# Performance work log

Hardware: AMD Instinct MI355X
Metric: run time of the kernel (lower is better)

Reference implementation:

```python
import jax, jax.numpy as jnp
import numpy as np

N, B, C, H = 2048, 2, 1024, 16
HD = C // H


def setup_inputs() -> dict:
    key = jax.random.key(0)
    ks = jax.random.split(key, 11)
    s = 0.02
    return {
        "query": jax.random.normal(ks[0], (N, B, C), jnp.float32),
        "key": jax.random.normal(ks[1], (N, B, C), jnp.float32),
        "value": jax.random.normal(ks[2], (B, N, C), jnp.float32),
        "num_heads": H,
        "Wq": jax.random.normal(ks[3], (C, C), jnp.float32) * s,
        "bq": jnp.zeros((C,), jnp.float32),
        "Wk": jax.random.normal(ks[4], (C, HD), jnp.float32) * s,
        "bk": jnp.zeros((HD,), jnp.float32),
        "Wv": jax.random.normal(ks[5], (C, HD), jnp.float32) * s,
        "bv": jnp.zeros((HD,), jnp.float32),
        "Wp": jax.random.normal(ks[6], (C, C), jnp.float32) * s,
        "bp": jnp.zeros((C,), jnp.float32),
    }


def reference(query, key, value, num_heads, Wq, bq, Wk, bk, Wv, bv, Wp, bp):
    # query/key arrive seq-first (N,B,C); permute to batch-first as in torch code
    k_in = jnp.transpose(key, (1, 0, 2))    # (B, Nk, C)
    q_in = jnp.transpose(query, (1, 0, 2))  # (B, Nq, C)
    Bsz, Nq, Cd = q_in.shape
    hd = Cd // num_heads
    scale = hd ** -0.5

    # shared single K/V head (MQA)
    k = k_in @ Wk + bk                      # (B, Nk, hd)
    v = value @ Wv + bv                     # (B, Nk, hd)
    q = (q_in @ Wq + bq).reshape(Bsz, Nq, num_heads, hd)
    q = jnp.transpose(q, (0, 2, 1, 3)) * scale  # (B, H, Nq, hd)

    attn = jnp.einsum('bhqd,bkd->bhqk', q, k)   # (B, H, Nq, Nk)
    attn = jax.nn.softmax(attn, axis=-1)
    x = jnp.einsum('bhqk,bkd->bhqd', attn, v)   # (B, H, Nq, hd)
    x = jnp.transpose(x, (0, 2, 1, 3)).reshape(Bsz, Nq, Cd)
    x = x @ Wp + bp
    return jnp.transpose(x, (1, 0, 2))          # (Nq, B, C)
```

## Files before the change

### kernel.cpp

```cpp
#include <hip/hip_runtime.h>
#include <hip/hip_bf16.h>

#define DI __device__ __forceinline__

typedef float f32x4 __attribute__((ext_vector_type(4)));
typedef float f32x16 __attribute__((ext_vector_type(16)));
typedef short s16x8 __attribute__((ext_vector_type(8)));
typedef unsigned short u16x4 __attribute__((ext_vector_type(4)));
typedef unsigned long long u64;


DI unsigned short f2bf(float x) {
  union { float f; unsigned u; } v; v.f = x;
  unsigned r = 0x7fffu + ((v.u >> 16) & 1u);
  return (unsigned short)((v.u + r) >> 16);
}

DI unsigned cvtpk(float lo, float hi) {
  unsigned u;
  asm("v_cvt_pk_bf16_f32 %0, %1, %2" : "=v"(u) : "v"(lo), "v"(hi));
  return u;
}

DI f32x16 zero16() {
  f32x16 z;
#pragma unroll
  for (int i = 0; i < 16; ++i) z[i] = 0.f;
  return z;
}

DI float max16(const f32x16& a) {
  float m0 = fmaxf(a[0], a[1]),  m1 = fmaxf(a[2], a[3]);
  float m2 = fmaxf(a[4], a[5]),  m3 = fmaxf(a[6], a[7]);
  float m4 = fmaxf(a[8], a[9]),  m5 = fmaxf(a[10], a[11]);
  float m6 = fmaxf(a[12], a[13]), m7 = fmaxf(a[14], a[15]);
  m0 = fmaxf(m0, m1); m2 = fmaxf(m2, m3); m4 = fmaxf(m4, m5); m6 = fmaxf(m6, m7);
  return fmaxf(fmaxf(m0, m2), fmaxf(m4, m6));
}

DI float sum16(const f32x16& a) {
  float s0 = a[0] + a[1],  s1 = a[2] + a[3];
  float s2 = a[4] + a[5],  s3 = a[6] + a[7];
  float s4 = a[8] + a[9],  s5 = a[10] + a[11];
  float s6 = a[12] + a[13], s7 = a[14] + a[15];
  s0 += s1; s2 += s3; s4 += s5; s6 += s7;
  return (s0 + s2) + (s4 + s6);
}

DI void gll16(const void* g, void* l) {
  __builtin_amdgcn_global_load_lds(
      (const __attribute__((address_space(1))) void*)g,
      (__attribute__((address_space(3))) void*)l, 16, 0, 0);
}

DI f32x16 mfma32(s16x8 a, s16x8 b, f32x16 c) {
  return __builtin_amdgcn_mfma_f32_32x32x16_bf16(a, b, c, 0, 0, 0);
}

DI f32x4 mfma16(s16x8 a, s16x8 b, f32x4 c) {
  return __builtin_amdgcn_mfma_f32_16x16x32_bf16(a, b, c, 0, 0, 0);
}

__global__ __launch_bounds__(256) void wconv_kernel(
    const float* __restrict__ Wq, const float* __restrict__ Wk,
    const float* __restrict__ Wv, const float* __restrict__ Wp,
    unsigned short* __restrict__ WqT, unsigned short* __restrict__ WkT,
    unsigned short* __restrict__ WvT, unsigned short* __restrict__ WpT)
{
  int bid = blockIdx.x;
  const float* W; unsigned short* WT; int Ncols; int base;
  if (bid < 512)       { W = Wq; WT = WqT; Ncols = 1024; base = bid; }
  else if (bid < 1024) { W = Wp; WT = WpT; Ncols = 1024; base = bid - 512; }
  else if (bid < 1056) { W = Wk; WT = WkT; Ncols = 64;   base = bid - 1024; }
  else                 { W = Wv; WT = WvT; Ncols = 64;   base = bid - 1056; }
  int nb = base >> 5, kb = base & 31;
  int n = nb * 64 + (threadIdx.x & 63);
  int k = kb * 32 + (threadIdx.x >> 6) * 8;
  float f[8];
#pragma unroll
  for (int i = 0; i < 8; ++i) f[i] = W[(size_t)(k + i) * Ncols + n];
  union { unsigned u[4]; s16x8 v; } x;
#pragma unroll
  for (int i = 0; i < 4; ++i) x.u[i] = cvtpk(f[2 * i], f[2 * i + 1]);
  *(s16x8*)(WT + (size_t)n * 1024 + k) = x.v;
}

__global__ __launch_bounds__(256) void cvt3_kernel(
    const float* __restrict__ q, const float* __restrict__ k,
    const float* __restrict__ v, unsigned short* __restrict__ qbf,
    unsigned short* __restrict__ kbf, unsigned short* __restrict__ vbf)
{
  int gid = blockIdx.x * 256 + threadIdx.x;
  int which = gid >> 19;
  int idx = gid & 524287;
  int row = idx >> 7;
  int c8 = (idx & 127) << 3;
  const float* src; unsigned short* dst; size_t soff;
  if (which == 0)      { src = q; dst = qbf; }
  else if (which == 1) { src = k; dst = kbf; }
  else                 { src = v; dst = vbf; }
  if (which < 2) {
    int b = row >> 11, n = row & 2047;
    soff = ((size_t)n * 2 + b) * 1024 + c8;
  } else {
    soff = (size_t)row * 1024 + c8;
  }
  f32x4 v0 = *(const f32x4*)(src + soff);
  f32x4 v1 = *(const f32x4*)(src + soff + 4);
  union { unsigned u[4]; s16x8 v; } x;
  x.u[0] = cvtpk(v0.x, v0.y); x.u[1] = cvtpk(v0.z, v0.w);
  x.u[2] = cvtpk(v1.x, v1.y); x.u[3] = cvtpk(v1.z, v1.w);
  *(s16x8*)(dst + (size_t)row * 1024 + c8) = x.v;
}

template<int BM, int BN, int MODE, int KSPLIT>
__global__ __launch_bounds__(256) void gemm16_kernel(
    const unsigned short* __restrict__ A1, const unsigned short* __restrict__ A2,
    const unsigned short* __restrict__ B1, const unsigned short* __restrict__ B2,
    const float* __restrict__ bias, void* __restrict__ Cpv, float scale)
{
  __shared__ unsigned short Asub[BM * 64];
  __shared__ unsigned short Bsub[BN * 64];

  const int tid = threadIdx.x;
  const int lane = tid & 63, wave = tid >> 6;
  const int l16 = lane & 15, kq = lane >> 4;
  const int wr = wave >> 1, wc = wave & 1;
  constexpr int WROWS = BM / 2, WCOLS = BN / 2;
  constexpr int MI = WROWS / 16, NJ = WCOLS / 16;

  const unsigned short* A = A1; const unsigned short* Bt = B1;
  int sel = 0;
  if constexpr (MODE == 1) {
    sel = blockIdx.y;
    if (sel) { A = A2; Bt = B2; }
  }
  const int row0 = blockIdx.x * BM;
  const int col0 = (MODE == 1) ? 0 : blockIdx.y * BN;
  const int kt0 = (KSPLIT > 1) ? blockIdx.z * (16 / KSPLIT) : 0;
  const int kt1 = kt0 + 16 / KSPLIT;

  f32x4 acc[MI][NJ];
#pragma unroll
  for (int mi = 0; mi < MI; ++mi)
#pragma unroll
    for (int nj = 0; nj < NJ; ++nj) acc[mi][nj] = f32x4{0.f, 0.f, 0.f, 0.f};

  for (int kt = kt0; kt < kt1; ++kt) {
    const int k0 = kt * 64;
    __syncthreads();
#pragma unroll
    for (int i = 0; i < BM / 32; ++i) {
      int o = i * 4096 + tid * 16;
      int r = o >> 7, c = (o & 127) >> 1;
      gll16(A + (size_t)(row0 + r) * 1024 + k0 + c,
            (char*)Asub + i * 4096 + wave * 1024);
    }
#pragma unroll
    for (int i = 0; i < BN / 32; ++i) {
      int o = i * 4096 + tid * 16;
      int r = o >> 7, c = (o & 127) >> 1;
      gll16(Bt + (size_t)(col0 + r) * 1024 + k0 + c,
            (char*)Bsub + i * 4096 + wave * 1024);
    }
    __syncthreads();
#pragma unroll
    for (int ks = 0; ks < 2; ++ks) {
      s16x8 af[MI]; s16x8 bfr[NJ];
#pragma unroll
      for (int mi = 0; mi < MI; ++mi)
        af[mi] = *(const s16x8*)(Asub + (wr * WROWS + mi * 16 + l16) * 64 + ks * 32 + kq * 8);
#pragma unroll
      for (int nj = 0; nj < NJ; ++nj)
        bfr[nj] = *(const s16x8*)(Bsub + (wc * WCOLS + nj * 16 + l16) * 64 + ks * 32 + kq * 8);
#pragma unroll
      for (int mi = 0; mi < MI; ++mi)
#pragma unroll
        for (int nj = 0; nj < NJ; ++nj)
          acc[mi][nj] = mfma16(af[mi], bfr[nj], acc[mi][nj]);
    }
  }

#pragma unroll
  for (int mi = 0; mi < MI; ++mi)
#pragma unroll
  for (int nj = 0; nj < NJ; ++nj) {
    int col = col0 + wc * WCOLS + nj * 16 + l16;
    int rowb = row0 + wr * WROWS + mi * 16 + kq * 4;
    float bv = (MODE == 1) ? 0.f : bias[col];
#pragma unroll
    for (int r = 0; r < 4; ++r) {
      int row = rowb + r;
      float val = acc[mi][nj][r] + bv;
      if constexpr (MODE == 0) {
        ((unsigned short*)Cpv)[(size_t)row * 1024 + col] = f2bf(val * scale);
      } else if constexpr (MODE == 1) {
        ((float*)Cpv)[(((size_t)blockIdx.z * 2 + sel) * 4096 + row) * 64 + col] = val;
      } else {
        ((float*)Cpv)[(size_t)(row & 2047) * 2048 + (size_t)(row >> 11) * 1024 + col] = val;
      }
    }
  }
}

__global__ __launch_bounds__(256) void kvreduce_kernel(
    const float* __restrict__ part, const float* __restrict__ bk,
    const float* __restrict__ bv, unsigned short* __restrict__ kproj,
    unsigned short* __restrict__ vprojT)
{
  int gid = blockIdx.x * 256 + threadIdx.x;
  int kv = gid >> 18;
  int rem = gid & 262143;
  int row = rem >> 6, col = rem & 63;
  float s = 0.f;
#pragma unroll
  for (int z = 0; z < 4; ++z)
    s += part[(((size_t)z * 2 + kv) * 4096 + row) * 64 + col];
  s += (kv ? bv : bk)[col];
  if (kv == 0)
    kproj[(size_t)row * 64 + col] = f2bf(s);
  else
    vprojT[(size_t)(row >> 11) * 131072 + (size_t)col * 2048 + (row & 2047)] = f2bf(s);
}

__global__ __launch_bounds__(512, 4) void attn_kernel(
    const unsigned short* __restrict__ qp, const unsigned short* __restrict__ kp,
    const unsigned short* __restrict__ vpt, unsigned short* __restrict__ xout)
{
  constexpr int KSTR = 72;
  __shared__ unsigned short SM[36864];
#define KBUF(c, hh) (SM + ((c) * 2 + (hh)) * (64 * KSTR))
#define VBUF(c, hh) (SM + 18432 + ((c) * 2 + (hh)) * (64 * KSTR))

  const int tid = threadIdx.x;
  const int lane = tid & 63, wave = tid >> 6;
  const int lq = lane & 31, hi = lane >> 5;
  const int qsub = wave & 3, half = wave >> 2;
  const int b = blockIdx.y >> 4, h = blockIdx.y & 15;
  const int q0 = blockIdx.x * 128 + qsub * 32;
  const size_t qrow = (size_t)(b * 2048 + q0 + lq);

  s16x8 qf[4];
#pragma unroll
  for (int s = 0; s < 4; ++s)
    qf[s] = *(const s16x8*)(qp + qrow * 1024 + h * 64 + s * 16 + hi * 8);

  f32x16 xacc0 = zero16(), xacc1 = zero16();
  float mrun = -1e30f, ssum = 0.f;

  const unsigned short* kb = kp + (size_t)b * (2048 * 64);
  const unsigned short* vb = vpt + (size_t)b * (64 * 2048);

  const int srow = tid >> 3;
  const int scol = (tid & 7) * 8;

  s16x8 kA, kB, vA, vB;
  {
    kA = *(const s16x8*)(kb + (size_t)srow * 64 + scol);
    kB = *(const s16x8*)(kb + (size_t)(16 * 64 + srow) * 64 + scol);
    vA = *(const s16x8*)(vb + (size_t)srow * 2048 + scol);
    vB = *(const s16x8*)(vb + (size_t)srow * 2048 + 16 * 64 + scol);
    *(s16x8*)(KBUF(0, 0) + srow * KSTR + scol) = kA;
    *(s16x8*)(KBUF(0, 1) + srow * KSTR + scol) = kB;
    *(s16x8*)(VBUF(0, 0) + srow * KSTR + scol) = vA;
    *(s16x8*)(VBUF(0, 1) + srow * KSTR + scol) = vB;
  }
  int cur = 0;

  for (int it = 0; it < 16; ++it) {
    __syncthreads();
    if (it + 1 < 16) {
      kA = *(const s16x8*)(kb + (size_t)((it + 1) * 64 + srow) * 64 + scol);
      kB = *(const s16x8*)(kb + (size_t)((it + 17) * 64 + srow) * 64 + scol);
      vA = *(const s16x8*)(vb + (size_t)srow * 2048 + (it + 1) * 64 + scol);
      vB = *(const s16x8*)(vb + (size_t)srow * 2048 + (it + 17) * 64 + scol);
    }
    const unsigned short* Kc = KBUF(cur, half);
    const unsigned short* Vc = VBUF(cur, half);

    f32x16 sacc0 = zero16(), sacc1 = zero16();
    __builtin_amdgcn_s_setprio(1);
#pragma unroll
    for (int s = 0; s < 4; ++s) {
      int c = s * 16 + hi * 8;
      s16x8 kf0 = *(const s16x8*)(Kc + lq * KSTR + c);
      s16x8 kf1 = *(const s16x8*)(Kc + (32 + lq) * KSTR + c);
      sacc0 = mfma32(kf0, qf[s], sacc0);
      sacc1 = mfma32(kf1, qf[s], sacc1);
    }
    __builtin_amdgcn_s_setprio(0);

    float tm = fmaxf(max16(sacc0), max16(sacc1));
    tm = fmaxf(tm, __shfl_xor(tm, 32));
    if (!__all(tm <= mrun + 8.f)) {
      float mnew = fmaxf(mrun, tm);
      float alpha = __builtin_amdgcn_exp2f(mrun - mnew);
      ssum *= alpha;
#pragma unroll
      for (int e = 0; e < 16; ++e) { xacc0[e] *= alpha; xacc1[e] *= alpha; }
      mrun = mnew;
    }
    f32x16 p0, p1;
#pragma unroll
    for (int e = 0; e < 16; ++e) p0[e] = __builtin_amdgcn_exp2f(sacc0[e] - mrun);
#pragma unroll
    for (int e = 0; e < 16; ++e) p1[e] = __builtin_amdgcn_exp2f(sacc1[e] - mrun);
    float tsum = sum16(p0) + sum16(p1);
    tsum += __shfl_xor(tsum, 32);
    ssum += tsum;

    s16x8 pb[4];
#pragma unroll
    for (int grp = 0; grp < 4; ++grp) {
      const f32x16& pp = (grp < 2) ? p0 : p1;
      const int eb = (grp & 1) * 8;
      unsigned A  = cvtpk(pp[eb + 0], pp[eb + 1]);
      unsigned Bw = cvtpk(pp[eb + 2], pp[eb + 3]);
      unsigned Cw = cvtpk(pp[eb + 4], pp[eb + 5]);
      unsigned Dw = cvtpk(pp[eb + 6], pp[eb + 7]);
      unsigned rA = (unsigned)__shfl_xor((int)(hi ? A : Cw), 32);
      unsigned rB = (unsigned)__shfl_xor((int)(hi ? Bw : Dw), 32);
      union { unsigned u[4]; s16x8 v; } pk_;
      pk_.u[0] = hi ? rA : A;
      pk_.u[1] = hi ? rB : Bw;
      pk_.u[2] = hi ? Cw : rA;
      pk_.u[3] = hi ? Dw : rB;
      pb[grp] = pk_.v;
    }

    __builtin_amdgcn_s_setprio(1);
#pragma unroll
    for (int kvs = 0; kvs < 4; ++kvs) {
      int c = kvs * 16 + hi * 8;
      s16x8 vf0 = *(const s16x8*)(Vc + lq * KSTR + c);
      s16x8 vf1 = *(const s16x8*)(Vc + (32 + lq) * KSTR + c);
      xacc0 = mfma32(vf0, pb[kvs], xacc0);
      xacc1 = mfma32(vf1, pb[kvs], xacc1);
    }
    __builtin_amdgcn_s_setprio(0);

    if (it + 1 < 16) {
      *(s16x8*)(KBUF(cur ^ 1, 0) + srow * KSTR + scol) = kA;
      *(s16x8*)(KBUF(cur ^ 1, 1) + srow * KSTR + scol) = kB;
      *(s16x8*)(VBUF(cur ^ 1, 0) + srow * KSTR + scol) = vA;
      *(s16x8*)(VBUF(cur ^ 1, 1) + srow * KSTR + scol) = vB;
      cur ^= 1;
    }
  }

  __syncthreads();
  float* msc = (float*)SM;
  const int mi_ = (qsub * 64 + lane) * 37;
  if (half == 1) {
#pragma unroll
    for (int e = 0; e < 16; ++e) { msc[mi_ + e] = xacc0[e]; msc[mi_ + 16 + e] = xacc1[e]; }
    msc[mi_ + 32] = mrun;
    msc[mi_ + 33] = ssum;
  }
  __syncthreads();
  if (half == 0) {
    float pm = msc[mi_ + 32], ps = msc[mi_ + 33];
    float mf = fmaxf(mrun, pm);
    float aa = __builtin_amdgcn_exp2f(mrun - mf);
    float bb = __builtin_amdgcn_exp2f(pm - mf);
    float inv = 1.0f / (ssum * aa + ps * bb);
#pragma unroll
    for (int dj = 0; dj < 2; ++dj) {
      const f32x16 xa = dj ? xacc1 : xacc0;
#pragma unroll
      for (int g = 0; g < 4; ++g) {
        u16x4 o4;
#pragma unroll
        for (int r = 0; r < 4; ++r) {
          int e = g * 4 + r;
          float merged = xa[e] * aa + msc[mi_ + dj * 16 + e] * bb;
          o4[r] = f2bf(merged * inv);
        }
        int d0 = dj * 32 + 8 * g + 4 * hi;
        *(u16x4*)(xout + qrow * 1024 + h * 64 + d0) = o4;
      }
    }
  }
#undef KBUF
#undef VBUF
}

extern "C" void kernel_launch(void* const* d_in, const int* in_sizes, int n_in,
                              void* d_out, int out_size, void* d_ws, size_t ws_size,
                              hipStream_t stream)
{
  const float* query = (const float*)d_in[0];
  const float* key   = (const float*)d_in[1];
  const float* value = (const float*)d_in[2];
  const float* Wq = (const float*)d_in[4];
  const float* bq = (const float*)d_in[5];
  const float* Wk = (const float*)d_in[6];
  const float* bk = (const float*)d_in[7];
  const float* Wv = (const float*)d_in[8];
  const float* bv = (const float*)d_in[9];
  const float* Wp = (const float*)d_in[10];
  const float* bp = (const float*)d_in[11];

  char* ws = (char*)d_ws;
  unsigned short* WqT    = (unsigned short*)(ws);
  unsigned short* WpT    = (unsigned short*)(ws + (2u << 20));
  unsigned short* WkT    = (unsigned short*)(ws + (4u << 20));
  unsigned short* WvT    = (unsigned short*)(ws + (4u << 20) + (128u << 10));
  unsigned short* kproj  = (unsigned short*)(ws + (5u << 20));
  unsigned short* vprojT = (unsigned short*)(ws + (5u << 20) + (512u << 10));
  unsigned short* qproj  = (unsigned short*)(ws + (6u << 20));
  unsigned short* xbuf   = (unsigned short*)(ws + (15u << 20));
  float*          part   = (float*)xbuf;
  unsigned short* vbf    = (unsigned short*)(ws + (24u << 20));
  unsigned short* qbf    = (unsigned short*)d_out;
  unsigned short* kbf    = (unsigned short*)d_out + 4194304;

  wconv_kernel<<<dim3(1088), 256, 0, stream>>>(Wq, Wk, Wv, Wp, WqT, WkT, WvT, WpT);
  cvt3_kernel<<<dim3(6144), 256, 0, stream>>>(query, key, value, qbf, kbf, vbf);

  const float qscale = 0.18033688011112042f;
  gemm16_kernel<64, 64, 0, 1><<<dim3(64, 16), 256, 0, stream>>>(
      qbf, qbf, WqT, WqT, bq, qproj, qscale);
  gemm16_kernel<64, 64, 1, 4><<<dim3(64, 2, 4), 256, 0, stream>>>(
      kbf, vbf, WkT, WvT, nullptr, part, 1.0f);
  kvreduce_kernel<<<dim3(2048), 256, 0, stream>>>(part, bk, bv, kproj, vprojT);
  attn_kernel<<<dim3(16, 32), 512, 0, stream>>>(qproj, kproj, vprojT, xbuf);
  gemm16_kernel<64, 64, 2, 1><<<dim3(64, 16), 256, 0, stream>>>(
      xbuf, xbuf, WpT, WpT, bp, d_out, 1.0f);
}
```

Measured before the change: 122.2 us.

## Fuse K/V bf16 conversion into KV GEMM, double-buffer GEMMs, retile attention

The separate fp32-to-bf16 conversion of key and value is removed. A new gemmkv_kernel loads fp32 activations, converts them in registers and writes them to LDS, with a register-prefetched double buffer. The Q and output projection GEMMs now use 128x64 tiles with double-buffered global_load_lds staging. The attention kernel processes 32 keys per iteration with a smaller LDS footprint so the occupancy hint can rise from 4 to 6 blocks. It also interleaves exp/pack with the PV MFMAs, uses v_max3 for the row max, and starts the running max at 0 instead of -1e30. That last change relies on the lazy-rescale threshold and adds some numeric risk if scores fall far below zero.

```diff
diff --git a/kernel.cpp b/kernel.cpp
--- a/kernel.cpp
+++ b/kernel.cpp
@@ -22,6 +22,12 @@
   return u;
 }
 
+DI float max3f(float a, float b, float c) {
+  float d;
+  asm("v_max3_f32 %0, %1, %2, %3" : "=v"(d) : "v"(a), "v"(b), "v"(c));
+  return d;
+}
+
 DI f32x16 zero16() {
   f32x16 z;
 #pragma unroll
@@ -29,22 +35,15 @@
   return z;
 }
 
-DI float max16(const f32x16& a) {
-  float m0 = fmaxf(a[0], a[1]),  m1 = fmaxf(a[2], a[3]);
-  float m2 = fmaxf(a[4], a[5]),  m3 = fmaxf(a[6], a[7]);
-  float m4 = fmaxf(a[8], a[9]),  m5 = fmaxf(a[10], a[11]);
-  float m6 = fmaxf(a[12], a[13]), m7 = fmaxf(a[14], a[15]);
-  m0 = fmaxf(m0, m1); m2 = fmaxf(m2, m3); m4 = fmaxf(m4, m5); m6 = fmaxf(m6, m7);
-  return fmaxf(fmaxf(m0, m2), fmaxf(m4, m6));
-}
-
-DI float sum16(const f32x16& a) {
-  float s0 = a[0] + a[1],  s1 = a[2] + a[3];
-  float s2 = a[4] + a[5],  s3 = a[6] + a[7];
-  float s4 = a[8] + a[9],  s5 = a[10] + a[11];
-  float s6 = a[12] + a[13], s7 = a[14] + a[15];
-  s0 += s1; s2 += s3; s4 += s5; s6 += s7;
-  return (s0 + s2) + (s4 + s6);
+DI float max16_3(const f32x16& a) {
+  float m0 = max3f(a[0], a[1], a[2]);
+  float m1 = max3f(a[3], a[4], a[5]);
+  float m2 = max3f(a[6], a[7], a[8]);
+  float m3 = max3f(a[9], a[10], a[11]);
+  float m4 = max3f(a[12], a[13], a[14]);
+  float n0 = max3f(m0, m1, m2);
+  float n1 = max3f(m3, m4, a[15]);
+  return fmaxf(n0, n1);
 }
 
 DI void gll16(const void* g, void* l) {
@@ -85,121 +84,196 @@
   *(s16x8*)(WT + (size_t)n * 1024 + k) = x.v;
 }
 
-__global__ __launch_bounds__(256) void cvt3_kernel(
-    const float* __restrict__ q, const float* __restrict__ k,
-    const float* __restrict__ v, unsigned short* __restrict__ qbf,
-    unsigned short* __restrict__ kbf, unsigned short* __restrict__ vbf)
+__global__ __launch_bounds__(256) void cvt1_kernel(
+    const float* __restrict__ q, unsigned short* __restrict__ qbf)
 {
   int gid = blockIdx.x * 256 + threadIdx.x;
-  int which = gid >> 19;
-  int idx = gid & 524287;
-  int row = idx >> 7;
-  int c8 = (idx & 127) << 3;
-  const float* src; unsigned short* dst; size_t soff;
-  if (which == 0)      { src = q; dst = qbf; }
-  else if (which == 1) { src = k; dst = kbf; }
-  else                 { src = v; dst = vbf; }
-  if (which < 2) {
-    int b = row >> 11, n = row & 2047;
-    soff = ((size_t)n * 2 + b) * 1024 + c8;
-  } else {
-    soff = (size_t)row * 1024 + c8;
-  }
-  f32x4 v0 = *(const f32x4*)(src + soff);
-  f32x4 v1 = *(const f32x4*)(src + soff + 4);
+  int row = gid >> 7;
+  int c8 = (gid & 127) << 3;
+  int b = row >> 11, n = row & 2047;
+  size_t soff = ((size_t)n * 2 + b) * 1024 + c8;
+  f32x4 v0 = *(const f32x4*)(q + soff);
+  f32x4 v1 = *(const f32x4*)(q + soff + 4);
   union { unsigned u[4]; s16x8 v; } x;
   x.u[0] = cvtpk(v0.x, v0.y); x.u[1] = cvtpk(v0.z, v0.w);
   x.u[2] = cvtpk(v1.x, v1.y); x.u[3] = cvtpk(v1.z, v1.w);
-  *(s16x8*)(dst + (size_t)row * 1024 + c8) = x.v;
-}
-
-template<int BM, int BN, int MODE, int KSPLIT>
+  *(s16x8*)(qbf + (size_t)row * 1024 + c8) = x.v;
+}
+
+template<int MODE>
 __global__ __launch_bounds__(256) void gemm16_kernel(
-    const unsigned short* __restrict__ A1, const unsigned short* __restrict__ A2,
-    const unsigned short* __restrict__ B1, const unsigned short* __restrict__ B2,
+    const unsigned short* __restrict__ A, const unsigned short* __restrict__ Bt,
     const float* __restrict__ bias, void* __restrict__ Cpv, float scale)
 {
-  __shared__ unsigned short Asub[BM * 64];
-  __shared__ unsigned short Bsub[BN * 64];
+  __shared__ __align__(16) unsigned short Asub[2][128 * 64];
+  __shared__ __align__(16) unsigned short Bsub[2][64 * 64];
 
   const int tid = threadIdx.x;
   const int lane = tid & 63, wave = tid >> 6;
   const int l16 = lane & 15, kq = lane >> 4;
   const int wr = wave >> 1, wc = wave & 1;
-  constexpr int WROWS = BM / 2, WCOLS = BN / 2;
-  constexpr int MI = WROWS / 16, NJ = WCOLS / 16;
-
-  const unsigned short* A = A1; const unsigned short* Bt = B1;
-  int sel = 0;
-  if constexpr (MODE == 1) {
-    sel = blockIdx.y;
-    if (sel) { A = A2; Bt = B2; }
-  }
-  const int row0 = blockIdx.x * BM;
-  const int col0 = (MODE == 1) ? 0 : blockIdx.y * BN;
-  const int kt0 = (KSPLIT > 1) ? blockIdx.z * (16 / KSPLIT) : 0;
-  const int kt1 = kt0 + 16 / KSPLIT;
-
-  f32x4 acc[MI][NJ];
-#pragma unroll
-  for (int mi = 0; mi < MI; ++mi)
-#pragma unroll
-    for (int nj = 0; nj < NJ; ++nj) acc[mi][nj] = f32x4{0.f, 0.f, 0.f, 0.f};
-
-  for (int kt = kt0; kt < kt1; ++kt) {
+  const int row0 = blockIdx.x * 128;
+  const int col0 = blockIdx.y * 64;
+
+  f32x4 acc[4][2];
+#pragma unroll
+  for (int mi = 0; mi < 4; ++mi)
+#pragma unroll
+    for (int nj = 0; nj < 2; ++nj) acc[mi][nj] = f32x4{0.f, 0.f, 0.f, 0.f};
+
+  auto STAGE = [&](int bf, int kt) {
     const int k0 = kt * 64;
-    __syncthreads();
-#pragma unroll
-    for (int i = 0; i < BM / 32; ++i) {
+#pragma unroll
+    for (int i = 0; i < 4; ++i) {
       int o = i * 4096 + tid * 16;
       int r = o >> 7, c = (o & 127) >> 1;
       gll16(A + (size_t)(row0 + r) * 1024 + k0 + c,
-            (char*)Asub + i * 4096 + wave * 1024);
-    }
-#pragma unroll
-    for (int i = 0; i < BN / 32; ++i) {
+            (char*)Asub[bf] + i * 4096 + wave * 1024);
+    }
+#pragma unroll
+    for (int i = 0; i < 2; ++i) {
       int o = i * 4096 + tid * 16;
       int r = o >> 7, c = (o & 127) >> 1;
       gll16(Bt + (size_t)(col0 + r) * 1024 + k0 + c,
-            (char*)Bsub + i * 4096 + wave * 1024);
+            (char*)Bsub[bf] + i * 4096 + wave * 1024);
+    }
+  };
+
+  STAGE(0, 0);
+  __syncthreads();
+  int cur = 0;
+  for (int kt = 0; kt < 16; ++kt) {
+    if (kt + 1 < 16) STAGE(cur ^ 1, kt + 1);
+#pragma unroll
+    for (int ks = 0; ks < 2; ++ks) {
+      s16x8 af[4]; s16x8 bf2[2];
+#pragma unroll
+      for (int mi = 0; mi < 4; ++mi)
+        af[mi] = *(const s16x8*)(Asub[cur] + (wr * 64 + mi * 16 + l16) * 64 + ks * 32 + kq * 8);
+#pragma unroll
+      for (int nj = 0; nj < 2; ++nj)
+        bf2[nj] = *(const s16x8*)(Bsub[cur] + (wc * 32 + nj * 16 + l16) * 64 + ks * 32 + kq * 8);
+#pragma unroll
+      for (int mi = 0; mi < 4; ++mi)
+#pragma unroll
+        for (int nj = 0; nj < 2; ++nj)
+          acc[mi][nj] = mfma16(af[mi], bf2[nj], acc[mi][nj]);
     }
     __syncthreads();
-#pragma unroll
-    for (int ks = 0; ks < 2; ++ks) {
-      s16x8 af[MI]; s16x8 bfr[NJ];
-#pragma unroll
-      for (int mi = 0; mi < MI; ++mi)
-        af[mi] = *(const s16x8*)(Asub + (wr * WROWS + mi * 16 + l16) * 64 + ks * 32 + kq * 8);
-#pragma unroll
-      for (int nj = 0; nj < NJ; ++nj)
-        bfr[nj] = *(const s16x8*)(Bsub + (wc * WCOLS + nj * 16 + l16) * 64 + ks * 32 + kq * 8);
-#pragma unroll
-      for (int mi = 0; mi < MI; ++mi)
-#pragma unroll
-        for (int nj = 0; nj < NJ; ++nj)
-          acc[mi][nj] = mfma16(af[mi], bfr[nj], acc[mi][nj]);
-    }
-  }
-
-#pragma unroll
-  for (int mi = 0; mi < MI; ++mi)
-#pragma unroll
-  for (int nj = 0; nj < NJ; ++nj) {
-    int col = col0 + wc * WCOLS + nj * 16 + l16;
-    int rowb = row0 + wr * WROWS + mi * 16 + kq * 4;
-    float bv = (MODE == 1) ? 0.f : bias[col];
+    cur ^= 1;
+  }
+
+#pragma unroll
+  for (int mi = 0; mi < 4; ++mi)
+#pragma unroll
+  for (int nj = 0; nj < 2; ++nj) {
+    int col = col0 + wc * 32 + nj * 16 + l16;
+    int rowb = row0 + wr * 64 + mi * 16 + kq * 4;
+    float bv = bias[col];
 #pragma unroll
     for (int r = 0; r < 4; ++r) {
       int row = rowb + r;
       float val = acc[mi][nj][r] + bv;
       if constexpr (MODE == 0) {
         ((unsigned short*)Cpv)[(size_t)row * 1024 + col] = f2bf(val * scale);
-      } else if constexpr (MODE == 1) {
-        ((float*)Cpv)[(((size_t)blockIdx.z * 2 + sel) * 4096 + row) * 64 + col] = val;
       } else {
         ((float*)Cpv)[(size_t)(row & 2047) * 2048 + (size_t)(row >> 11) * 1024 + col] = val;
       }
     }
+  }
+}
+
+__global__ __launch_bounds__(256) void gemmkv_kernel(
+    const float* __restrict__ Akey, const float* __restrict__ Aval,
+    const unsigned short* __restrict__ Wk, const unsigned short* __restrict__ Wv,
+    float* __restrict__ part)
+{
+  __shared__ __align__(16) unsigned short Asub[2][64 * 64];
+  __shared__ __align__(16) unsigned short Bsub[2][64 * 64];
+
+  const int tid = threadIdx.x;
+  const int lane = tid & 63, wave = tid >> 6;
+  const int l16 = lane & 15, kq = lane >> 4;
+  const int wr = wave >> 1, wc = wave & 1;
+  const int sel = blockIdx.y;
+  const float* Af = sel ? Aval : Akey;
+  const unsigned short* Bt = sel ? Wv : Wk;
+  const int row0 = blockIdx.x * 64;
+  const int kt0 = blockIdx.z * 4, kt1 = kt0 + 4;
+
+  const int ar = tid >> 2, ac = (tid & 3) * 16;
+  const int gm = row0 + ar;
+  const size_t grow = sel ? (size_t)gm * 1024
+                          : (size_t)((gm & 2047) * 2 + (gm >> 11)) * 1024;
+
+  auto LOADA = [&](int kt, f32x4* a4) {
+#pragma unroll
+    for (int i = 0; i < 4; ++i)
+      a4[i] = *(const f32x4*)(Af + grow + kt * 64 + ac + i * 4);
+  };
+  auto WRITEA = [&](int bf, const f32x4* a4) {
+    union { unsigned u[8]; s16x8 v[2]; } x;
+#pragma unroll
+    for (int i = 0; i < 4; ++i) {
+      x.u[2 * i]     = cvtpk(a4[i].x, a4[i].y);
+      x.u[2 * i + 1] = cvtpk(a4[i].z, a4[i].w);
+    }
+    *(s16x8*)(Asub[bf] + ar * 64 + ac)     = x.v[0];
+    *(s16x8*)(Asub[bf] + ar * 64 + ac + 8) = x.v[1];
+  };
+  auto STAGEB = [&](int bf, int kt) {
+#pragma unroll
+    for (int i = 0; i < 2; ++i) {
+      int o = i * 4096 + tid * 16;
+      int r = o >> 7, c = (o & 127) >> 1;
+      gll16(Bt + (size_t)r * 1024 + kt * 64 + c,
+            (char*)Bsub[bf] + i * 4096 + wave * 1024);
+    }
+  };
+
+  f32x4 acc[2][2];
+#pragma unroll
+  for (int mi = 0; mi < 2; ++mi)
+#pragma unroll
+    for (int nj = 0; nj < 2; ++nj) acc[mi][nj] = f32x4{0.f, 0.f, 0.f, 0.f};
+
+  f32x4 a4[4];
+  LOADA(kt0, a4);
+  STAGEB(0, kt0);
+  WRITEA(0, a4);
+  __syncthreads();
+  int cur = 0;
+  for (int kt = kt0; kt < kt1; ++kt) {
+    if (kt + 1 < kt1) { LOADA(kt + 1, a4); STAGEB(cur ^ 1, kt + 1); }
+#pragma unroll
+    for (int ks = 0; ks < 2; ++ks) {
+      s16x8 af[2]; s16x8 bf2[2];
+#pragma unroll
+      for (int mi = 0; mi < 2; ++mi)
+        af[mi] = *(const s16x8*)(Asub[cur] + (wr * 32 + mi * 16 + l16) * 64 + ks * 32 + kq * 8);
+#pragma unroll
+      for (int nj = 0; nj < 2; ++nj)
+        bf2[nj] = *(const s16x8*)(Bsub[cur] + (wc * 32 + nj * 16 + l16) * 64 + ks * 32 + kq * 8);
+#pragma unroll
+      for (int mi = 0; mi < 2; ++mi)
+#pragma unroll
+        for (int nj = 0; nj < 2; ++nj)
+          acc[mi][nj] = mfma16(af[mi], bf2[nj], acc[mi][nj]);
+    }
+    if (kt + 1 < kt1) WRITEA(cur ^ 1, a4);
+    __syncthreads();
+    cur ^= 1;
+  }
+
+#pragma unroll
+  for (int mi = 0; mi < 2; ++mi)
+#pragma unroll
+  for (int nj = 0; nj < 2; ++nj) {
+    int col = wc * 32 + nj * 16 + l16;
+    int rowb = row0 + wr * 32 + mi * 16 + kq * 4;
+#pragma unroll
+    for (int r = 0; r < 4; ++r)
+      part[(((size_t)blockIdx.z * 2 + sel) * 4096 + rowb + r) * 64 + col] = acc[mi][nj][r];
   }
 }
 
@@ -223,14 +297,13 @@
     vprojT[(size_t)(row >> 11) * 131072 + (size_t)col * 2048 + (row & 2047)] = f2bf(s);
 }
 
-__global__ __launch_bounds__(512, 4) void attn_kernel(
+__global__ __launch_bounds__(512, 6) void attn_kernel(
     const unsigned short* __restrict__ qp, const unsigned short* __restrict__ kp,
     const unsigned short* __restrict__ vpt, unsigned short* __restrict__ xout)
 {
-  constexpr int KSTR = 72;
-  __shared__ unsigned short SM[36864];
-#define KBUF(c, hh) (SM + ((c) * 2 + (hh)) * (64 * KSTR))
-#define VBUF(c, hh) (SM + 18432 + ((c) * 2 + (hh)) * (64 * KSTR))
+  __shared__ __align__(16) unsigned short SM[19456];
+#define KOFF(c, hh) (SM + (c) * 9728 + (hh) * 2304)
+#define VOFF(c, hh) (SM + (c) * 9728 + 4608 + (hh) * 2560)
 
   const int tid = threadIdx.x;
   const int lane = tid & 63, wave = tid >> 6;
@@ -246,51 +319,42 @@
     qf[s] = *(const s16x8*)(qp + qrow * 1024 + h * 64 + s * 16 + hi * 8);
 
   f32x16 xacc0 = zero16(), xacc1 = zero16();
-  float mrun = -1e30f, ssum = 0.f;
-
-  const unsigned short* kb = kp + (size_t)b * (2048 * 64);
-  const unsigned short* vb = vpt + (size_t)b * (64 * 2048);
-
-  const int srow = tid >> 3;
-  const int scol = (tid & 7) * 8;
-
-  s16x8 kA, kB, vA, vB;
-  {
-    kA = *(const s16x8*)(kb + (size_t)srow * 64 + scol);
-    kB = *(const s16x8*)(kb + (size_t)(16 * 64 + srow) * 64 + scol);
-    vA = *(const s16x8*)(vb + (size_t)srow * 2048 + scol);
-    vB = *(const s16x8*)(vb + (size_t)srow * 2048 + 16 * 64 + scol);
-    *(s16x8*)(KBUF(0, 0) + srow * KSTR + scol) = kA;
-    *(s16x8*)(KBUF(0, 1) + srow * KSTR + scol) = kB;
-    *(s16x8*)(VBUF(0, 0) + srow * KSTR + scol) = vA;
-    *(s16x8*)(VBUF(0, 1) + srow * KSTR + scol) = vB;
-  }
+  float mrun = 0.f, ssum = 0.f;
+
+  const int sh = tid >> 8;
+  const int kidx = tid & 255;
+  const int krow = kidx >> 3, kcol = (kidx & 7) * 8;
+  const int vrow = kidx >> 2, vcol = (kidx & 3) * 8;
+  const unsigned short* kg = kp + (size_t)b * (2048 * 64) + (size_t)(sh * 1024 + krow) * 64 + kcol;
+  const unsigned short* vg = vpt + (size_t)b * (64 * 2048) + (size_t)vrow * 2048 + sh * 1024 + vcol;
+  unsigned short* kd0 = KOFF(0, sh) + krow * 72 + kcol;
+  unsigned short* vd0 = VOFF(0, sh) + vrow * 40 + vcol;
+
+  s16x8 kr = *(const s16x8*)kg;
+  s16x8 vr = *(const s16x8*)vg;
+  *(s16x8*)kd0 = kr;
+  *(s16x8*)vd0 = vr;
   int cur = 0;
 
-  for (int it = 0; it < 16; ++it) {
+  for (int it = 0; it < 32; ++it) {
     __syncthreads();
-    if (it + 1 < 16) {
-      kA = *(const s16x8*)(kb + (size_t)((it + 1) * 64 + srow) * 64 + scol);
-      kB = *(const s16x8*)(kb + (size_t)((it + 17) * 64 + srow) * 64 + scol);
-      vA = *(const s16x8*)(vb + (size_t)srow * 2048 + (it + 1) * 64 + scol);
-      vB = *(const s16x8*)(vb + (size_t)srow * 2048 + (it + 17) * 64 + scol);
-    }
-    const unsigned short* Kc = KBUF(cur, half);
-    const unsigned short* Vc = VBUF(cur, half);
-
-    f32x16 sacc0 = zero16(), sacc1 = zero16();
+    if (it + 1 < 32) {
+      kr = *(const s16x8*)(kg + (size_t)(it + 1) * 2048);
+      vr = *(const s16x8*)(vg + (it + 1) * 32);
+    }
+    const unsigned short* Kc = KOFF(cur, half);
+    const unsigned short* Vc = VOFF(cur, half);
+
+    f32x16 sacc = zero16();
     __builtin_amdgcn_s_setprio(1);
 #pragma unroll
     for (int s = 0; s < 4; ++s) {
-      int c = s * 16 + hi * 8;
-      s16x8 kf0 = *(const s16x8*)(Kc + lq * KSTR + c);
-      s16x8 kf1 = *(const s16x8*)(Kc + (32 + lq) * KSTR + c);
-      sacc0 = mfma32(kf0, qf[s], sacc0);
-      sacc1 = mfma32(kf1, qf[s], sacc1);
+      s16x8 kf = *(const s16x8*)(Kc + lq * 72 + s * 16 + hi * 8);
+      sacc = mfma32(kf, qf[s], sacc);
     }
     __builtin_amdgcn_s_setprio(0);
 
-    float tm = fmaxf(max16(sacc0), max16(sacc1));
+    float tm = max16_3(sacc);
     tm = fmaxf(tm, __shfl_xor(tm, 32));
     if (!__all(tm <= mrun + 8.f)) {
       float mnew = fmaxf(mrun, tm);
@@ -300,24 +364,24 @@
       for (int e = 0; e < 16; ++e) { xacc0[e] *= alpha; xacc1[e] *= alpha; }
       mrun = mnew;
     }
-    f32x16 p0, p1;
-#pragma unroll
-    for (int e = 0; e < 16; ++e) p0[e] = __builtin_amdgcn_exp2f(sacc0[e] - mrun);
-#pragma unroll
-    for (int e = 0; e < 16; ++e) p1[e] = __builtin_amdgcn_exp2f(sacc1[e] - mrun);
-    float tsum = sum16(p0) + sum16(p1);
-    tsum += __shfl_xor(tsum, 32);
-    ssum += tsum;
-
-    s16x8 pb[4];
-#pragma unroll
-    for (int grp = 0; grp < 4; ++grp) {
-      const f32x16& pp = (grp < 2) ? p0 : p1;
-      const int eb = (grp & 1) * 8;
-      unsigned A  = cvtpk(pp[eb + 0], pp[eb + 1]);
-      unsigned Bw = cvtpk(pp[eb + 2], pp[eb + 3]);
-      unsigned Cw = cvtpk(pp[eb + 4], pp[eb + 5]);
-      unsigned Dw = cvtpk(pp[eb + 6], pp[eb + 7]);
+
+    __builtin_amdgcn_s_setprio(1);
+#pragma unroll
+    for (int g = 0; g < 2; ++g) {
+      const int eb = g * 8;
+      float p0 = __builtin_amdgcn_exp2f(sacc[eb + 0] - mrun);
+      float p1 = __builtin_amdgcn_exp2f(sacc[eb + 1] - mrun);
+      float p2 = __builtin_amdgcn_exp2f(sacc[eb + 2] - mrun);
+      float p3 = __builtin_amdgcn_exp2f(sacc[eb + 3] - mrun);
+      float p4 = __builtin_amdgcn_exp2f(sacc[eb + 4] - mrun);
+      float p5 = __builtin_amdgcn_exp2f(sacc[eb + 5] - mrun);
+      float p6 = __builtin_amdgcn_exp2f(sacc[eb + 6] - mrun);
+      float p7 = __builtin_amdgcn_exp2f(sacc[eb + 7] - mrun);
+      ssum += ((p0 + p1) + (p2 + p3)) + ((p4 + p5) + (p6 + p7));
+      unsigned A  = cvtpk(p0, p1);
+      unsigned Bw = cvtpk(p2, p3);
+      unsigned Cw = cvtpk(p4, p5);
+      unsigned Dw = cvtpk(p6, p7);
       unsigned rA = (unsigned)__shfl_xor((int)(hi ? A : Cw), 32);
       unsigned rB = (unsigned)__shfl_xor((int)(hi ? Bw : Dw), 32);
       union { unsigned u[4]; s16x8 v; } pk_;
@@ -325,28 +389,20 @@
       pk_.u[1] = hi ? rB : Bw;
       pk_.u[2] = hi ? Cw : rA;
       pk_.u[3] = hi ? Dw : rB;
-      pb[grp] = pk_.v;
-    }
-
-    __builtin_amdgcn_s_setprio(1);
-#pragma unroll
-    for (int kvs = 0; kvs < 4; ++kvs) {
-      int c = kvs * 16 + hi * 8;
-      s16x8 vf0 = *(const s16x8*)(Vc + lq * KSTR + c);
-      s16x8 vf1 = *(const s16x8*)(Vc + (32 + lq) * KSTR + c);
-      xacc0 = mfma32(vf0, pb[kvs], xacc0);
-      xacc1 = mfma32(vf1, pb[kvs], xacc1);
+      s16x8 vf0 = *(const s16x8*)(Vc + lq * 40 + g * 16 + hi * 8);
+      s16x8 vf1 = *(const s16x8*)(Vc + (32 + lq) * 40 + g * 16 + hi * 8);
+      xacc0 = mfma32(vf0, pk_.v, xacc0);
+      xacc1 = mfma32(vf1, pk_.v, xacc1);
     }
     __builtin_amdgcn_s_setprio(0);
 
-    if (it + 1 < 16) {
-      *(s16x8*)(KBUF(cur ^ 1, 0) + srow * KSTR + scol) = kA;
-      *(s16x8*)(KBUF(cur ^ 1, 1) + srow * KSTR + scol) = kB;
-      *(s16x8*)(VBUF(cur ^ 1, 0) + srow * KSTR + scol) = vA;
-      *(s16x8*)(VBUF(cur ^ 1, 1) + srow * KSTR + scol) = vB;
+    if (it + 1 < 32) {
+      *(s16x8*)(kd0 + (cur ^ 1) * 9728) = kr;
+      *(s16x8*)(vd0 + (cur ^ 1) * 9728) = vr;
       cur ^= 1;
     }
   }
+  ssum += __shfl_xor(ssum, 32);
 
   __syncthreads();
   float* msc = (float*)SM;
@@ -381,8 +437,8 @@
       }
     }
   }
-#undef KBUF
-#undef VBUF
+#undef KOFF
+#undef VOFF
 }
 
 extern "C" void kernel_launch(void* const* d_in, const int* in_sizes, int n_in,
@@ -411,20 +467,15 @@
   unsigned short* qproj  = (unsigned short*)(ws + (6u << 20));
   unsigned short* xbuf   = (unsigned short*)(ws + (15u << 20));
   float*          part   = (float*)xbuf;
-  unsigned short* vbf    = (unsigned short*)(ws + (24u << 20));
   unsigned short* qbf    = (unsigned short*)d_out;
-  unsigned short* kbf    = (unsigned short*)d_out + 4194304;
 
   wconv_kernel<<<dim3(1088), 256, 0, stream>>>(Wq, Wk, Wv, Wp, WqT, WkT, WvT, WpT);
-  cvt3_kernel<<<dim3(6144), 256, 0, stream>>>(query, key, value, qbf, kbf, vbf);
+  cvt1_kernel<<<dim3(2048), 256, 0, stream>>>(query, qbf);
 
   const float qscale = 0.18033688011112042f;
-  gemm16_kernel<64, 64, 0, 1><<<dim3(64, 16), 256, 0, stream>>>(
-      qbf, qbf, WqT, WqT, bq, qproj, qscale);
-  gemm16_kernel<64, 64, 1, 4><<<dim3(64, 2, 4), 256, 0, stream>>>(
-      kbf, vbf, WkT, WvT, nullptr, part, 1.0f);
+  gemm16_kernel<0><<<dim3(32, 16), 256, 0, stream>>>(qbf, WqT, bq, qproj, qscale);
+  gemmkv_kernel<<<dim3(64, 2, 4), 256, 0, stream>>>(key, value, WkT, WvT, part);
   kvreduce_kernel<<<dim3(2048), 256, 0, stream>>>(part, bk, bv, kproj, vprojT);
   attn_kernel<<<dim3(16, 32), 512, 0, stream>>>(qproj, kproj, vprojT, xbuf);
-  gemm16_kernel<64, 64, 2, 1><<<dim3(64, 16), 256, 0, stream>>>(
-      xbuf, xbuf, WpT, WpT, bp, d_out, 1.0f);
-}
+  gemm16_kernel<2><<<dim3(32, 16), 256, 0, stream>>>(xbuf, WpT, bp, d_out, 1.0f);
+}
```

After: 240.7 us. 97.0% more time.
